# Optimization experiments

Hardware: AMD Instinct MI355X
Metric: run time of the kernel (lower is better)

## Reference

```python
import jax, jax.numpy as jnp
import numpy as np

RADIUS = 0.1
MAX_NEIGHBORS = 64


def setup_inputs() -> dict:
    key0 = jax.random.key(0)
    k1, k2 = jax.random.split(key0)
    query = jax.random.uniform(k1, (4, 2048, 3), dtype=jnp.float32)
    key = jax.random.uniform(k2, (4, 8192, 3), dtype=jnp.float32)
    return {"query": query, "key": key}


def reference(query, key):
    # PointNet++-style ball query: for each query point, the indices of the
    # first MAX_NEIGHBORS key points (in key order) with squared distance
    # < RADIUS^2; remaining slots are padded with the first found neighbor
    # index (0 if no neighbor exists, matching zero-initialized CUDA output).
    B, N1, _ = query.shape
    N2 = key.shape[1]
    K = MAX_NEIGHBORS

    # [B, N1, N2] squared pairwise distances
    d2 = jnp.sum((query[:, :, None, :] - key[:, None, :, :]) ** 2, axis=-1)
    within = d2 < jnp.float32(RADIUS) ** 2  # [B, N1, N2] bool

    # slot each valid neighbor lands in (in key-index order)
    pos = jnp.cumsum(within.astype(jnp.int32), axis=-1) - 1  # [B, N1, N2]
    take = within & (pos < K)
    slot = jnp.where(take, pos, K)  # invalid entries routed to dummy slot K

    n2_idx = jnp.broadcast_to(jnp.arange(N2, dtype=jnp.int32), (B, N1, N2))
    b_idx = jnp.arange(B)[:, None, None]
    n1_idx = jnp.arange(N1)[None, :, None]

    out = jnp.full((B, N1, K + 1), -1, dtype=jnp.int32)
    # slots < K are unique per (b, n1); duplicates only at dummy slot K
    out = out.at[b_idx, n1_idx, slot].set(n2_idx)
    out = out[..., :K]  # drop dummy slot

    # pad empty slots with index of first in-radius neighbor (0 if none)
    first = jnp.argmax(within, axis=-1).astype(jnp.int32)  # [B, N1]
    out = jnp.where(out < 0, first[..., None], out)
    return out
```

## Files before the change

kernel.cpp:

```cpp
#include <hip/hip_runtime.h>


constexpr int   K    = 64;
constexpr float R2   = 0.01f;
constexpr int   B    = 4;
constexpr int   N1   = 2048;
constexpr int   N2   = 8192;
constexpr int   GC   = 5;
constexpr int   NCELL = GC * GC * GC;
constexpr float INVCELL = 5.0f;

constexpr size_t SORTED_BYTES = (size_t)B * N2 * 16;
constexpr size_t WS_NEEDED    = SORTED_BYTES + (size_t)(B * NCELL * 2 + B * (NCELL + 1)) * 4;

__device__ __forceinline__ int cell_of(float v) {
    int c = (int)(v * INVCELL);
    return c < 0 ? 0 : (c > GC - 1 ? GC - 1 : c);
}

__global__ __launch_bounds__(256) void zero_kernel(int* __restrict__ z, int n) {
    for (int i = threadIdx.x; i < n; i += 256) z[i] = 0;
}

__global__ __launch_bounds__(256) void hist_kernel(
    const float* __restrict__ key, int* __restrict__ counts)
{
    const int p = blockIdx.x * 256 + threadIdx.x;
    const int b = p >> 13;
    const float x = key[p * 3 + 0];
    const float y = key[p * 3 + 1];
    const float z = key[p * 3 + 2];
    const int cell = (cell_of(x) * GC + cell_of(y)) * GC + cell_of(z);
    atomicAdd(&counts[b * NCELL + cell], 1);
}

__global__ __launch_bounds__(128) void scan_kernel(
    const int* __restrict__ counts, int* __restrict__ cell_start)
{
    __shared__ int sbuf[128];
    const int t = threadIdx.x;
    const int b = blockIdx.x;
    int v = (t < NCELL) ? counts[b * NCELL + t] : 0;
    sbuf[t] = v;
    __syncthreads();
    for (int off = 1; off < 128; off <<= 1) {
        int x = (t >= off) ? sbuf[t - off] : 0;
        __syncthreads();
        sbuf[t] += x;
        __syncthreads();
    }
    if (t < NCELL) cell_start[b * (NCELL + 1) + t + 1] = sbuf[t];
    if (t == 0)    cell_start[b * (NCELL + 1)] = 0;
}

__global__ __launch_bounds__(256) void scatter_kernel(
    const float* __restrict__ key, const int* __restrict__ cell_start,
    int* __restrict__ counters, float4* __restrict__ sorted)
{
    const int p = blockIdx.x * 256 + threadIdx.x;
    const int b = p >> 13;
    const int i = p & (N2 - 1);
    const float x = key[p * 3 + 0];
    const float y = key[p * 3 + 1];
    const float z = key[p * 3 + 2];
    const int cell = (cell_of(x) * GC + cell_of(y)) * GC + cell_of(z);
    const int ofs  = atomicAdd(&counters[b * NCELL + cell], 1);
    const int pos  = cell_start[b * (NCELL + 1) + cell] + ofs;
    float4 v;
    v.x = x; v.y = y; v.z = z; v.w = __int_as_float(i);
    sorted[b * N2 + pos] = v;
}

__global__ __launch_bounds__(256) void ballquery_grid_kernel(
    const float* __restrict__ query,
    const float4* __restrict__ sorted,
    const int* __restrict__ cell_start,
    int* __restrict__ out)
{
    __shared__ unsigned int bm[4 * 256];

    const int lane = threadIdx.x & 63;
    const int wv   = threadIdx.x >> 6;
    const int q    = blockIdx.x * 4 + wv;
    const int b    = q >> 11;

    const float qx = query[q * 3 + 0];
    const float qy = query[q * 3 + 1];
    const float qz = query[q * 3 + 2];

    const float ux = qx * INVCELL, uy = qy * INVCELL, uz = qz * INVCELL;
    const int cx = cell_of(qx), cy = cell_of(qy), cz = cell_of(qz);
    const int nx = (ux - cx < 0.5f) ? cx - 1 : cx + 1;
    const int ny = (uy - cy < 0.5f) ? cy - 1 : cy + 1;
    const int nz = (uz - cz < 0.5f) ? cz - 1 : cz + 1;
    const int xlo = max(0, min(cx, nx)), xhi = min(GC - 1, max(cx, nx));
    const int ylo = max(0, min(cy, ny)), yhi = min(GC - 1, max(cy, ny));
    const int zlo = max(0, min(cz, nz)), zhi = min(GC - 1, max(cz, nz));

    unsigned int* wbm = bm + wv * 256;
    uint4 zz; zz.x = zz.y = zz.z = zz.w = 0u;
    ((uint4*)wbm)[lane] = zz;
    __threadfence_block();

    const int*    cs = cell_start + b * (NCELL + 1);
    const float4* sb = sorted + b * N2;

    for (int xx = xlo; xx <= xhi; ++xx) {
        for (int yy = ylo; yy <= yhi; ++yy) {
            const int colz = (xx * GC + yy) * GC;
            const int s = cs[colz + zlo];
            const int e = cs[colz + zhi + 1];
            for (int t0 = s; t0 < e; t0 += 64) {
                const int i = t0 + lane;
                const float4 kv = sb[min(i, e - 1)];
                const float dx = kv.x - qx;
                const float dy = kv.y - qy;
                const float dz = kv.z - qz;
                const bool within = (i < e) && (dx * dx + dy * dy + dz * dz < R2);
                if (within) {
                    const int id = __float_as_int(kv.w);
                    atomicOr(&wbm[id >> 5], 1u << (id & 31));
                }
            }
        }
    }
    __threadfence_block();

    const uint4 w = ((const uint4*)wbm)[lane];
    const int c = __popc(w.x) + __popc(w.y) + __popc(w.z) + __popc(w.w);

    int x = c;
    #pragma unroll
    for (int off = 1; off < 64; off <<= 1) {
        int y = __shfl_up(x, off);
        if (lane >= off) x += y;
    }
    const int base = x - c;
    const int cnt  = __shfl(x, 63);

    int fs;
    if      (w.x) fs = __builtin_ctz(w.x);
    else if (w.y) fs = 32 + __builtin_ctz(w.y);
    else if (w.z) fs = 64 + __builtin_ctz(w.z);
    else if (w.w) fs = 96 + __builtin_ctz(w.w);
    else          fs = 0;
    int myfirst = c ? (lane << 7) + fs : 0x7fffffff;
    #pragma unroll
    for (int off = 32; off; off >>= 1)
        myfirst = min(myfirst, __shfl_xor(myfirst, off));
    const int firstIdx = (cnt == 0) ? 0 : myfirst;

    int* op = out + q * K;
    int slot = base;
    unsigned int wr[4] = {w.x, w.y, w.z, w.w};
    #pragma unroll
    for (int r = 0; r < 4; ++r) {
        unsigned int m = wr[r];
        const int bb = (lane << 7) + (r << 5);
        while (m) {
            const int bp = __builtin_ctz(m);
            m &= m - 1;
            if (slot < K) op[slot] = bb + bp;
            ++slot;
        }
    }

    const int kpad = cnt < K ? cnt : K;
    const int s2 = kpad + lane;
    if (s2 < K) op[s2] = firstIdx;
}

__global__ __launch_bounds__(256) void ballquery_bruteforce_kernel(
    const float* __restrict__ query, const float* __restrict__ key,
    int* __restrict__ out)
{
    const int lane = threadIdx.x & 63;
    const int q = blockIdx.x * 4 + (threadIdx.x >> 6);
    const int b = q >> 11;
    const float qx = query[q * 3], qy = query[q * 3 + 1], qz = query[q * 3 + 2];
    const float* kb = key + (size_t)b * N2 * 3;
    int* op = out + (size_t)q * K;
    int count = 0, first = 0;
    bool have_first = false;
    const unsigned long long lane_mask_lt = (lane == 0) ? 0ull : (~0ull >> (64 - lane));
    for (int c = 0; c < N2 / 64; ++c) {
        if (count >= K) break;
        const int j = (c << 6) + lane;
        const float* kp = kb + j * 3;
        const float dx = kp[0] - qx, dy = kp[1] - qy, dz = kp[2] - qz;
        const bool within = dx * dx + dy * dy + dz * dz < R2;
        const unsigned long long mask = __ballot(within);
        if (mask) {
            if (!have_first) { first = (c << 6) + __builtin_ctzll(mask); have_first = true; }
            if (within) {
                const int slot = count + __popcll(mask & lane_mask_lt);
                if (slot < K) op[slot] = j;
            }
            count += __popcll(mask);
        }
    }
    const int cnt = count < K ? count : K;
    if (cnt + lane < K) op[cnt + lane] = first;
}

extern "C" void kernel_launch(void* const* d_in, const int* in_sizes, int n_in,
                              void* d_out, int out_size, void* d_ws, size_t ws_size,
                              hipStream_t stream) {
    const float* query = (const float*)d_in[0];
    const float* key   = (const float*)d_in[1];
    int* out = (int*)d_out;

    if (ws_size < WS_NEEDED) {
        ballquery_bruteforce_kernel<<<(B * N1) / 4, 256, 0, stream>>>(query, key, out);
        return;
    }

    float4* sorted     = (float4*)d_ws;
    int*    counts     = (int*)((char*)d_ws + SORTED_BYTES);
    int*    counters   = counts + B * NCELL;
    int*    cell_start = counters + B * NCELL;

    zero_kernel<<<1, 256, 0, stream>>>(counts, B * NCELL * 2);
    hist_kernel<<<(B * N2) / 256, 256, 0, stream>>>(key, counts);
    scan_kernel<<<B, 128, 0, stream>>>(counts, cell_start);
    scatter_kernel<<<(B * N2) / 256, 256, 0, stream>>>(key, cell_start, counters, sorted);
    ballquery_grid_kernel<<<(B * N1) / 4, 256, 0, stream>>>(query, sorted, cell_start, out);
}
```

Baseline: 84.55 us.

## Fuse grid build into single per-batch kernel with shared-memory histogram

Replaces the four-kernel grid construction (zero, histogram, scan, scatter) with one kernel per batch that builds the histogram in shared memory, scans it, and scatters keys using shared-memory atomics. This removes three kernel launches and the global atomics and round trips through global memory for counts. In exchange the build runs on only 4 blocks of 1024 threads, so it uses far less of the GPU in parallel.

```diff
diff --git a/kernel.cpp b/kernel.cpp
--- a/kernel.cpp
+++ b/kernel.cpp
@@ -11,64 +11,72 @@
 constexpr float INVCELL = 5.0f;
 
 constexpr size_t SORTED_BYTES = (size_t)B * N2 * 16;
-constexpr size_t WS_NEEDED    = SORTED_BYTES + (size_t)(B * NCELL * 2 + B * (NCELL + 1)) * 4;
+constexpr size_t WS_NEEDED    = SORTED_BYTES + (size_t)(B * (NCELL + 1)) * 4;
 
 __device__ __forceinline__ int cell_of(float v) {
     int c = (int)(v * INVCELL);
     return c < 0 ? 0 : (c > GC - 1 ? GC - 1 : c);
 }
 
-__global__ __launch_bounds__(256) void zero_kernel(int* __restrict__ z, int n) {
-    for (int i = threadIdx.x; i < n; i += 256) z[i] = 0;
-}
-
-__global__ __launch_bounds__(256) void hist_kernel(
-    const float* __restrict__ key, int* __restrict__ counts)
+__global__ __launch_bounds__(1024) void build_kernel(
+    const float* __restrict__ key,
+    float4* __restrict__ sorted,
+    int* __restrict__ cell_start)
 {
-    const int p = blockIdx.x * 256 + threadIdx.x;
-    const int b = p >> 13;
-    const float x = key[p * 3 + 0];
-    const float y = key[p * 3 + 1];
-    const float z = key[p * 3 + 2];
-    const int cell = (cell_of(x) * GC + cell_of(y)) * GC + cell_of(z);
-    atomicAdd(&counts[b * NCELL + cell], 1);
-}
-
-__global__ __launch_bounds__(128) void scan_kernel(
-    const int* __restrict__ counts, int* __restrict__ cell_start)
-{
+    __shared__ int hist[NCELL];
     __shared__ int sbuf[128];
+    __shared__ int start[NCELL + 1];
+
+    const int b = blockIdx.x;
     const int t = threadIdx.x;
-    const int b = blockIdx.x;
-    int v = (t < NCELL) ? counts[b * NCELL + t] : 0;
-    sbuf[t] = v;
+    constexpr int PER = N2 / 1024;
+
+    if (t < NCELL) hist[t] = 0;
+    __syncthreads();
+
+    const float* kb = key + (size_t)b * N2 * 3;
+    int mycell[PER];
+    #pragma unroll
+    for (int r = 0; r < PER; ++r) {
+        const int i = r * 1024 + t;
+        const float x = kb[i * 3 + 0];
+        const float y = kb[i * 3 + 1];
+        const float z = kb[i * 3 + 2];
+        const int cell = (cell_of(x) * GC + cell_of(y)) * GC + cell_of(z);
+        mycell[r] = cell;
+        atomicAdd(&hist[cell], 1);
+    }
+    __syncthreads();
+
+    if (t < 128) sbuf[t] = (t < NCELL) ? hist[t] : 0;
     __syncthreads();
     for (int off = 1; off < 128; off <<= 1) {
-        int x = (t >= off) ? sbuf[t - off] : 0;
+        int v = 0;
+        if (t < 128 && t >= off) v = sbuf[t - off];
         __syncthreads();
-        sbuf[t] += x;
+        if (t < 128) sbuf[t] += v;
         __syncthreads();
     }
-    if (t < NCELL) cell_start[b * (NCELL + 1) + t + 1] = sbuf[t];
-    if (t == 0)    cell_start[b * (NCELL + 1)] = 0;
-}
-
-__global__ __launch_bounds__(256) void scatter_kernel(
-    const float* __restrict__ key, const int* __restrict__ cell_start,
-    int* __restrict__ counters, float4* __restrict__ sorted)
-{
-    const int p = blockIdx.x * 256 + threadIdx.x;
-    const int b = p >> 13;
-    const int i = p & (N2 - 1);
-    const float x = key[p * 3 + 0];
-    const float y = key[p * 3 + 1];
-    const float z = key[p * 3 + 2];
-    const int cell = (cell_of(x) * GC + cell_of(y)) * GC + cell_of(z);
-    const int ofs  = atomicAdd(&counters[b * NCELL + cell], 1);
-    const int pos  = cell_start[b * (NCELL + 1) + cell] + ofs;
-    float4 v;
-    v.x = x; v.y = y; v.z = z; v.w = __int_as_float(i);
-    sorted[b * N2 + pos] = v;
+    if (t < NCELL) start[t + 1] = sbuf[t];
+    if (t == 0)    start[0] = 0;
+    __syncthreads();
+    if (t < NCELL + 1) cell_start[b * (NCELL + 1) + t] = start[t];
+    if (t < NCELL)     hist[t] = start[t];
+    __syncthreads();
+
+    float4* sb = sorted + (size_t)b * N2;
+    #pragma unroll
+    for (int r = 0; r < PER; ++r) {
+        const int i = r * 1024 + t;
+        const int cell = mycell[r];
+        const int pos = atomicAdd(&hist[cell], 1);
+        float4 v;
+        v.x = kb[i * 3 + 0];
+        v.y = kb[i * 3 + 1];
+        v.z = kb[i * 3 + 2];
+        v.w = __int_as_float(i);
+        sb[pos] = v;
+    }
 }
 
 __global__ __launch_bounds__(256) void ballquery_grid_kernel(
@@ -103,7 +111,7 @@
     __threadfence_block();
 
     const int*    cs = cell_start + b * (NCELL + 1);
-    const float4* sb = sorted + b * N2;
+    const float4* sb = sorted + (size_t)b * N2;
 
     for (int xx = xlo; xx <= xhi; ++xx) {
         for (int yy = ylo; yy <= yhi; ++yy) {
@@ -216,13 +224,8 @@
     }
 
     float4* sorted     = (float4*)d_ws;
-    int*    counts     = (int*)((char*)d_ws + SORTED_BYTES);
-    int*    counters   = counts + B * NCELL;
-    int*    cell_start = counters + B * NCELL;
-
-    zero_kernel<<<1, 256, 0, stream>>>(counts, B * NCELL * 2);
-    hist_kernel<<<(B * N2) / 256, 256, 0, stream>>>(key, counts);
-    scan_kernel<<<B, 128, 0, stream>>>(counts, cell_start);
-    scatter_kernel<<<(B * N2) / 256, 256, 0, stream>>>(key, cell_start, counters, sorted);
+    int*    cell_start = (int*)((char*)d_ws + SORTED_BYTES);
+
+    build_kernel<<<B, 1024, 0, stream>>>(key, sorted, cell_start);
     ballquery_grid_kernel<<<(B * N1) / 4, 256, 0, stream>>>(query, sorted, cell_start, out);
 }
```

Measured after the change: 74.40 us. 1.14x faster.

## Merge grid build into two kernels using per-block shared-memory histograms

Applied to the files above, without the earlier changes.

Replaces the zero/hist/scan/scatter four-kernel grid build with two kernels. Each block builds a local histogram in shared memory and writes it out. The scatter kernel then recomputes the per-batch prefix sums and per-block offsets redundantly, and places points with shared-memory atomics. This removes two kernel launches and the global atomics, at the cost of redundant scan work in every scatter block. Ordering within a cell is now nondeterministic but is still covered by the bitmap step.

```diff
diff --git a/kernel.cpp b/kernel.cpp
--- a/kernel.cpp
+++ b/kernel.cpp
@@ -9,66 +9,91 @@
 constexpr int   GC   = 5;
 constexpr int   NCELL = GC * GC * GC;
 constexpr float INVCELL = 5.0f;
+constexpr int   SUBS       = 128;
+constexpr int   SUBS_PER_B = 32;
 
 constexpr size_t SORTED_BYTES = (size_t)B * N2 * 16;
-constexpr size_t WS_NEEDED    = SORTED_BYTES + (size_t)(B * NCELL * 2 + B * (NCELL + 1)) * 4;
+constexpr size_t CS_BYTES     = (size_t)B * (NCELL + 1) * 4;
+constexpr size_t WS_NEEDED    = SORTED_BYTES + CS_BYTES + (size_t)SUBS * NCELL * 4;
 
 __device__ __forceinline__ int cell_of(float v) {
     int c = (int)(v * INVCELL);
     return c < 0 ? 0 : (c > GC - 1 ? GC - 1 : c);
 }
 
-__global__ __launch_bounds__(256) void zero_kernel(int* __restrict__ z, int n) {
-    for (int i = threadIdx.x; i < n; i += 256) z[i] = 0;
-}
-
 __global__ __launch_bounds__(256) void hist_kernel(
-    const float* __restrict__ key, int* __restrict__ counts)
-{
-    const int p = blockIdx.x * 256 + threadIdx.x;
-    const int b = p >> 13;
+    const float* __restrict__ key,
+    int* __restrict__ hists)
+{
+    __shared__ int h[NCELL];
+    const int k = blockIdx.x;
+    const int t = threadIdx.x;
+    if (t < NCELL) h[t] = 0;
+    __syncthreads();
+    const int p = k * 256 + t;
     const float x = key[p * 3 + 0];
     const float y = key[p * 3 + 1];
     const float z = key[p * 3 + 2];
     const int cell = (cell_of(x) * GC + cell_of(y)) * GC + cell_of(z);
-    atomicAdd(&counts[b * NCELL + cell], 1);
-}
-
-__global__ __launch_bounds__(128) void scan_kernel(
-    const int* __restrict__ counts, int* __restrict__ cell_start)
+    atomicAdd(&h[cell], 1);
+    __syncthreads();
+    if (t < NCELL) hists[k * NCELL + t] = h[t];
+}
+
+__global__ __launch_bounds__(256) void scatter_kernel(
+    const float* __restrict__ key,
+    const int* __restrict__ hists,
+    int* __restrict__ cell_start,
+    float4* __restrict__ sorted)
 {
     __shared__ int sbuf[128];
+    __shared__ int cursor[NCELL];
+
+    const int k = blockIdx.x;
+    const int b = k >> 5;
+    const int s = k & 31;
     const int t = threadIdx.x;
-    const int b = blockIdx.x;
-    int v = (t < NCELL) ? counts[b * NCELL + t] : 0;
-    sbuf[t] = v;
+
+    int mybase = 0, total = 0;
+    if (t < NCELL) {
+        const int* hb = hists + (b * SUBS_PER_B) * NCELL + t;
+        int acc = 0;
+        #pragma unroll
+        for (int s2 = 0; s2 < SUBS_PER_B; ++s2) {
+            if (s2 == s) mybase = acc;
+            acc += hb[s2 * NCELL];
+        }
+        total = acc;
+    }
+
+    if (t < 128) sbuf[t] = (t < NCELL) ? total : 0;
     __syncthreads();
     for (int off = 1; off < 128; off <<= 1) {
-        int x = (t >= off) ? sbuf[t - off] : 0;
+        int v = 0;
+        if (t < 128 && t >= off) v = sbuf[t - off];
         __syncthreads();
-        sbuf[t] += x;
+        if (t < 128) sbuf[t] += v;
         __syncthreads();
     }
-    if (t < NCELL) cell_start[b * (NCELL + 1) + t + 1] = sbuf[t];
-    if (t == 0)    cell_start[b * (NCELL + 1)] = 0;
-}
-
-__global__ __launch_bounds__(256) void scatter_kernel(
-    const float* __restrict__ key, const int* __restrict__ cell_start,
-    int* __restrict__ counters, float4* __restrict__ sorted)
-{
-    const int p = blockIdx.x * 256 + threadIdx.x;
-    const int b = p >> 13;
-    const int i = p & (N2 - 1);
+    if (t < NCELL) {
+        const int excl = sbuf[t] - total;
+        cursor[t] = excl + mybase;
+        if (s == 0) {
+            cell_start[b * (NCELL + 1) + t + 1] = sbuf[t];
+            if (t == 0) cell_start[b * (NCELL + 1)] = 0;
+        }
+    }
+    __syncthreads();
+
+    const int p = k * 256 + t;
     const float x = key[p * 3 + 0];
     const float y = key[p * 3 + 1];
     const float z = key[p * 3 + 2];
     const int cell = (cell_of(x) * GC + cell_of(y)) * GC + cell_of(z);
-    const int ofs  = atomicAdd(&counters[b * NCELL + cell], 1);
-    const int pos  = cell_start[b * (NCELL + 1) + cell] + ofs;
+    const int pos  = atomicAdd(&cursor[cell], 1);
     float4 v;
-    v.x = x; v.y = y; v.z = z; v.w = __int_as_float(i);
-    sorted[b * N2 + pos] = v;
+    v.x = x; v.y = y; v.z = z; v.w = __int_as_float(p & (N2 - 1));
+    sorted[(size_t)b * N2 + pos] = v;
 }
 
 __global__ __launch_bounds__(256) void ballquery_grid_kernel(
@@ -103,7 +128,7 @@
     __threadfence_block();
 
     const int*    cs = cell_start + b * (NCELL + 1);
-    const float4* sb = sorted + b * N2;
+    const float4* sb = sorted + (size_t)b * N2;
 
     for (int xx = xlo; xx <= xhi; ++xx) {
         for (int yy = ylo; yy <= yhi; ++yy) {
@@ -216,13 +241,10 @@
     }
 
     float4* sorted     = (float4*)d_ws;
-    int*    counts     = (int*)((char*)d_ws + SORTED_BYTES);
-    int*    counters   = counts + B * NCELL;
-    int*    cell_start = counters + B * NCELL;
-
-    zero_kernel<<<1, 256, 0, stream>>>(counts, B * NCELL * 2);
-    hist_kernel<<<(B * N2) / 256, 256, 0, stream>>>(key, counts);
-    scan_kernel<<<B, 128, 0, stream>>>(counts, cell_start);
-    scatter_kernel<<<(B * N2) / 256, 256, 0, stream>>>(key, cell_start, counters, sorted);
+    int*    cell_start = (int*)((char*)d_ws + SORTED_BYTES);
+    int*    hists      = (int*)((char*)d_ws + SORTED_BYTES + CS_BYTES);
+
+    hist_kernel<<<SUBS, 256, 0, stream>>>(key, hists);
+    scatter_kernel<<<SUBS, 256, 0, stream>>>(key, hists, cell_start, sorted);
     ballquery_grid_kernel<<<(B * N1) / 4, 256, 0, stream>>>(query, sorted, cell_start, out);
 }
```

Result: faster. 68.71 us (-18.7%).

## Replace counting-sort grid build with fixed-capacity per-cell slabs

Applied to the files above, without the earlier changes.

The zero, histogram, scan and scatter kernels are replaced by a memset and a single build kernel. That kernel appends each key point into a fixed-capacity slab of 256 float4 entries per cell, using an atomic cursor. The query kernel then walks each neighbouring cell's slab separately, using the cursor count as the length. This removes two kernel launches and a full pass over the keys. In exchange, the query loop splits what used to be one contiguous z-range into per-cell runs with more partially filled wavefronts. Points that land in a cell beyond 256 entries are silently dropped, so correctness depends on the cells never overflowing.

```diff
diff --git a/kernel.cpp b/kernel.cpp
--- a/kernel.cpp
+++ b/kernel.cpp
@@ -9,53 +9,20 @@
 constexpr int   GC   = 5;
 constexpr int   NCELL = GC * GC * GC;
 constexpr float INVCELL = 5.0f;
+constexpr int   CAP  = 256;
 
-constexpr size_t SORTED_BYTES = (size_t)B * N2 * 16;
-constexpr size_t WS_NEEDED    = SORTED_BYTES + (size_t)(B * NCELL * 2 + B * (NCELL + 1)) * 4;
+constexpr size_t SLAB_BYTES = (size_t)B * NCELL * CAP * 16;
+constexpr size_t WS_NEEDED  = SLAB_BYTES + (size_t)B * NCELL * 4;
 
 __device__ __forceinline__ int cell_of(float v) {
     int c = (int)(v * INVCELL);
     return c < 0 ? 0 : (c > GC - 1 ? GC - 1 : c);
 }
 
-__global__ __launch_bounds__(256) void zero_kernel(int* __restrict__ z, int n) {
-    for (int i = threadIdx.x; i < n; i += 256) z[i] = 0;
-}
-
-__global__ __launch_bounds__(256) void hist_kernel(
-    const float* __restrict__ key, int* __restrict__ counts)
-{
-    const int p = blockIdx.x * 256 + threadIdx.x;
-    const int b = p >> 13;
-    const float x = key[p * 3 + 0];
-    const float y = key[p * 3 + 1];
-    const float z = key[p * 3 + 2];
-    const int cell = (cell_of(x) * GC + cell_of(y)) * GC + cell_of(z);
-    atomicAdd(&counts[b * NCELL + cell], 1);
-}
-
-__global__ __launch_bounds__(128) void scan_kernel(
-    const int* __restrict__ counts, int* __restrict__ cell_start)
-{
-    __shared__ int sbuf[128];
-    const int t = threadIdx.x;
-    const int b = blockIdx.x;
-    int v = (t < NCELL) ? counts[b * NCELL + t] : 0;
-    sbuf[t] = v;
-    __syncthreads();
-    for (int off = 1; off < 128; off <<= 1) {
-        int x = (t >= off) ? sbuf[t - off] : 0;
-        __syncthreads();
-        sbuf[t] += x;
-        __syncthreads();
-    }
-    if (t < NCELL) cell_start[b * (NCELL + 1) + t + 1] = sbuf[t];
-    if (t == 0)    cell_start[b * (NCELL + 1)] = 0;
-}
-
-__global__ __launch_bounds__(256) void scatter_kernel(
-    const float* __restrict__ key, const int* __restrict__ cell_start,
-    int* __restrict__ counters, float4* __restrict__ sorted)
+__global__ __launch_bounds__(256) void build_kernel(
+    const float* __restrict__ key,
+    float4* __restrict__ slab,
+    int* __restrict__ cursors)
 {
     const int p = blockIdx.x * 256 + threadIdx.x;
     const int b = p >> 13;
@@ -64,17 +31,18 @@
     const float y = key[p * 3 + 1];
     const float z = key[p * 3 + 2];
     const int cell = (cell_of(x) * GC + cell_of(y)) * GC + cell_of(z);
-    const int ofs  = atomicAdd(&counters[b * NCELL + cell], 1);
-    const int pos  = cell_start[b * (NCELL + 1) + cell] + ofs;
-    float4 v;
-    v.x = x; v.y = y; v.z = z; v.w = __int_as_float(i);
-    sorted[b * N2 + pos] = v;
+    const int pos  = atomicAdd(&cursors[b * NCELL + cell], 1);
+    if (pos < CAP) {
+        float4 v;
+        v.x = x; v.y = y; v.z = z; v.w = __int_as_float(i);
+        slab[(size_t)(b * NCELL + cell) * CAP + pos] = v;
+    }
 }
 
-__global__ __launch_bounds__(256) void ballquery_grid_kernel(
+__global__ __launch_bounds__(256) void query_kernel(
     const float* __restrict__ query,
-    const float4* __restrict__ sorted,
-    const int* __restrict__ cell_start,
+    const float4* __restrict__ slab,
+    const int* __restrict__ cursors,
     int* __restrict__ out)
 {
     __shared__ unsigned int bm[4 * 256];
@@ -98,28 +66,31 @@
     const int zlo = max(0, min(cz, nz)), zhi = min(GC - 1, max(cz, nz));
 
     unsigned int* wbm = bm + wv * 256;
-    uint4 zz; zz.x = zz.y = zz.z = zz.w = 0u;
-    ((uint4*)wbm)[lane] = zz;
+    uint4 zz4; zz4.x = zz4.y = zz4.z = zz4.w = 0u;
+    ((uint4*)wbm)[lane] = zz4;
     __threadfence_block();
 
-    const int*    cs = cell_start + b * (NCELL + 1);
-    const float4* sb = sorted + b * N2;
+    const int*    cb = cursors + b * NCELL;
+    const float4* sb = slab + (size_t)b * NCELL * CAP;
 
     for (int xx = xlo; xx <= xhi; ++xx) {
         for (int yy = ylo; yy <= yhi; ++yy) {
-            const int colz = (xx * GC + yy) * GC;
-            const int s = cs[colz + zlo];
-            const int e = cs[colz + zhi + 1];
-            for (int t0 = s; t0 < e; t0 += 64) {
-                const int i = t0 + lane;
-                const float4 kv = sb[min(i, e - 1)];
-                const float dx = kv.x - qx;
-                const float dy = kv.y - qy;
-                const float dz = kv.z - qz;
-                const bool within = (i < e) && (dx * dx + dy * dy + dz * dz < R2);
-                if (within) {
-                    const int id = __float_as_int(kv.w);
-                    atomicOr(&wbm[id >> 5], 1u << (id & 31));
+            for (int zz = zlo; zz <= zhi; ++zz) {
+                const int cid = (xx * GC + yy) * GC + zz;
+                const int cnt = min(cb[cid], CAP);
+                const float4* run = sb + (size_t)cid * CAP;
+                for (int t0 = 0; t0 < cnt; t0 += 64) {
+                    const int i = t0 + lane;
+                    const float4 kv = run[min(i, cnt - 1)];
+                    const float dx = kv.x - qx;
+                    const float dy = kv.y - qy;
+                    const float dz = kv.z - qz;
+                    const bool within = (i < cnt) &&
+                        (dx * dx + dy * dy + dz * dz < R2);
+                    if (within) {
+                        const int id = __float_as_int(kv.w);
+                        atomicOr(&wbm[id >> 5], 1u << (id & 31));
+                    }
                 }
             }
         }
@@ -215,14 +186,10 @@
         return;
     }
 
-    float4* sorted     = (float4*)d_ws;
-    int*    counts     = (int*)((char*)d_ws + SORTED_BYTES);
-    int*    counters   = counts + B * NCELL;
-    int*    cell_start = counters + B * NCELL;
+    float4* slab    = (float4*)d_ws;
+    int*    cursors = (int*)((char*)d_ws + SLAB_BYTES);
 
-    zero_kernel<<<1, 256, 0, stream>>>(counts, B * NCELL * 2);
-    hist_kernel<<<(B * N2) / 256, 256, 0, stream>>>(key, counts);
-    scan_kernel<<<B, 128, 0, stream>>>(counts, cell_start);
-    scatter_kernel<<<(B * N2) / 256, 256, 0, stream>>>(key, cell_start, counters, sorted);
-    ballquery_grid_kernel<<<(B * N1) / 4, 256, 0, stream>>>(query, sorted, cell_start, out);
+    hipMemsetAsync(cursors, 0, (size_t)B * NCELL * 4, stream);
+    build_kernel<<<(B * N2) / 256, 256, 0, stream>>>(key, slab, cursors);
+    query_kernel<<<(B * N1) / 4, 256, 0, stream>>>(query, slab, cursors, out);
 }
```

New measurement: 76.40 us. -9.6%, faster.
